# Performance work log

Hardware: AMD Instinct MI355X
Metric: run time of the kernel (lower is better)

The kernel has to match this reference:

```python
import jax, jax.numpy as jnp
import numpy as np

B, S, D, E = 8, 1024, 768, 8
F = 4 * D  # 3072


def setup_inputs() -> dict:
    key = jax.random.key(0)
    ks = jax.random.split(key, 5)
    scale = 0.02
    x = jax.random.normal(ks[0], (B, S, D), jnp.float32)
    gate_w = jax.random.normal(ks[1], (D, E), jnp.float32) * scale
    gate_b = jnp.zeros((E,), jnp.float32)
    w1 = jax.random.normal(ks[2], (E, D, F), jnp.float32) * scale
    b1 = jnp.zeros((E, F), jnp.float32)
    w2 = jax.random.normal(ks[3], (E, F, D), jnp.float32) * scale
    b2 = jnp.zeros((E, D), jnp.float32)
    return {"x": x, "gate_w": gate_w, "gate_b": gate_b,
            "w1": w1, "b1": b1, "w2": w2, "b2": b2}


def reference(x, gate_w, gate_b, w1, b1, w2, b2):
    # x: [B, S, D] -> tokens [T, D]
    orig_shape = x.shape
    xt = x.reshape(-1, x.shape[-1])  # [T, D]
    gates = jax.nn.softmax(xt @ gate_w + gate_b, axis=-1)  # [T, E]
    # original takes topk(k=2) but only uses indices[:, 0] == argmax (top-1)
    expert_idx = jnp.argmax(gates, axis=-1)  # [T]
    # NOTE: original does NOT scale expert output by gate probability.
    out = jnp.zeros_like(xt)
    n_experts = w1.shape[0]
    for e in range(n_experts):  # small fixed expert loop
        h = jax.nn.gelu(xt @ w1[e] + b1[e], approximate=False)  # [T, F]
        y = h @ w2[e] + b2[e]  # [T, D]
        out = jnp.where((expert_idx == e)[:, None], y, out)
    return out.reshape(orig_shape)
```

## Files before the change

### kernel.cpp

```cpp
#include <hip/hip_runtime.h>
#include <hip/hip_bf16.h>
#include <cstdint>
#include <cstddef>

static constexpr int T_TOK = 8192;
static constexpr int D_DIM = 768;
static constexpr int E_NUM = 8;
static constexpr int F_DIM = 3072;
static constexpr int MAX_TILES = 72;

typedef __attribute__((ext_vector_type(8))) short short8;
typedef __attribute__((ext_vector_type(4))) float floatx4;
typedef __attribute__((ext_vector_type(8))) unsigned short ushort8v;

__device__ __forceinline__ void async16(const void* g, void* l) {
  __builtin_amdgcn_global_load_lds(
      (const __attribute__((address_space(1))) unsigned int*)g,
      (__attribute__((address_space(3))) unsigned int*)l, 16, 0, 0);
}

__device__ __forceinline__ float gelu_fast(float v) {
  float s = v * (1.5957691f + 0.071354813f * v * v);
  return v / (1.0f + __expf(-s));
}

__global__ __launch_bounds__(256)
void gate_kernel(const float* __restrict__ x, const float* __restrict__ gw,
                 const float* __restrict__ gb, int* __restrict__ expert_idx,
                 __hip_bfloat16* __restrict__ xb) {
  int gid = blockIdx.x * blockDim.x + threadIdx.x;
  int tok = gid >> 6;
  int lane = threadIdx.x & 63;
  if (tok >= T_TOK) return;
  const float* xr = x + (size_t)tok * D_DIM;
  __hip_bfloat16* xbr = xb + (size_t)tok * D_DIM;
  float acc[8];
#pragma unroll
  for (int e = 0; e < 8; e++) acc[e] = 0.f;
#pragma unroll
  for (int i = 0; i < D_DIM / 64; i++) {
    int d = lane + i * 64;
    float v = xr[d];
    xbr[d] = __float2bfloat16(v);
    const float4* g4 = (const float4*)(gw + (size_t)d * 8);
    float4 a = g4[0], b = g4[1];
    acc[0] += v * a.x; acc[1] += v * a.y; acc[2] += v * a.z; acc[3] += v * a.w;
    acc[4] += v * b.x; acc[5] += v * b.y; acc[6] += v * b.z; acc[7] += v * b.w;
  }
#pragma unroll
  for (int e = 0; e < 8; e++) {
#pragma unroll
    for (int o = 32; o > 0; o >>= 1) acc[e] += __shfl_xor(acc[e], o, 64);
  }
  if (lane == 0) {
    int best = 0;
    float bv = acc[0] + gb[0];
#pragma unroll
    for (int e = 1; e < 8; e++) {
      float v = acc[e] + gb[e];
      if (v > bv) { bv = v; best = e; }
    }
    expert_idx[tok] = best;
  }
}

__global__ __launch_bounds__(256)
void count_kernel(const int* __restrict__ expert_idx, int* __restrict__ counts) {
  __shared__ int h[E_NUM];
  if (threadIdx.x < E_NUM) h[threadIdx.x] = 0;
  __syncthreads();
  int t = blockIdx.x * blockDim.x + threadIdx.x;
  if (t < T_TOK) atomicAdd(&h[expert_idx[t]], 1);
  __syncthreads();
  if (threadIdx.x < E_NUM && h[threadIdx.x] > 0)
    atomicAdd(&counts[threadIdx.x], h[threadIdx.x]);
}

__global__ void offsets_kernel(const int* __restrict__ counts, int* __restrict__ offs,
                               int* __restrict__ meta) {
  if (threadIdx.x == 0) {
    int s = 0, tc = 0;
    for (int e = 0; e < E_NUM; e++) {
      offs[e] = s;
      int cnt = counts[e];
      for (int m = 0; m * 128 < cnt; m++) {
        meta[1 + tc] = e;
        meta[1 + MAX_TILES + tc] = m;
        tc++;
      }
      s += cnt;
    }
    offs[E_NUM] = s;
    meta[0] = tc;
  }
}

__global__ __launch_bounds__(256)
void scatter_kernel(const int* __restrict__ expert_idx, const int* __restrict__ offs,
                    int* __restrict__ fill, int* __restrict__ perm) {
  __shared__ int lcnt[E_NUM];
  __shared__ int lbase[E_NUM];
  if (threadIdx.x < E_NUM) lcnt[threadIdx.x] = 0;
  __syncthreads();
  int t = blockIdx.x * blockDim.x + threadIdx.x;
  int e = -1, rank = 0;
  if (t < T_TOK) {
    e = expert_idx[t];
    rank = atomicAdd(&lcnt[e], 1);
  }
  __syncthreads();
  if (threadIdx.x < E_NUM)
    lbase[threadIdx.x] = (lcnt[threadIdx.x] > 0)
                           ? atomicAdd(&fill[threadIdx.x], lcnt[threadIdx.x]) : 0;
  __syncthreads();
  if (t < T_TOK) perm[offs[e] + lbase[e] + rank] = t;
}

__global__ __launch_bounds__(256)
void transpose_bf16(const float* __restrict__ in, __hip_bfloat16* __restrict__ out,
                    int R, int C) {
  __shared__ float t[64][65];
  const float* src = in + (size_t)blockIdx.z * R * C;
  __hip_bfloat16* dst = out + (size_t)blockIdx.z * R * C;
  int r0 = blockIdx.y * 64, c0 = blockIdx.x * 64;
  int tx = threadIdx.x & 15;
  int ty = threadIdx.x >> 4;
#pragma unroll
  for (int p = 0; p < 4; p++) {
    int r = ty + p * 16;
    float4 v = *(const float4*)&src[(size_t)(r0 + r) * C + c0 + tx * 4];
    t[tx * 4 + 0][r] = v.x; t[tx * 4 + 1][r] = v.y;
    t[tx * 4 + 2][r] = v.z; t[tx * 4 + 3][r] = v.w;
  }
  __syncthreads();
  int j = threadIdx.x & 7;
#pragma unroll
  for (int p = 0; p < 2; p++) {
    int cc = (threadIdx.x >> 3) + p * 32;
    __align__(16) __hip_bfloat16 tmp[8];
#pragma unroll
    for (int i = 0; i < 8; i++) tmp[i] = __float2bfloat16(t[cc][j * 8 + i]);
    *(ushort8v*)&dst[(size_t)(c0 + cc) * R + r0 + j * 8] = *(const ushort8v*)tmp;
  }
}

template<int K, int N, bool FIRST>
__global__ __launch_bounds__(256)
void moe_gemm(const __hip_bfloat16* __restrict__ A,
              const __hip_bfloat16* __restrict__ Bt,
              const float* __restrict__ bias,
              const int* __restrict__ meta,
              const int* __restrict__ offs,
              const int* __restrict__ perm,
              void* __restrict__ OutP) {
  int g = blockIdx.x;
  int xcd = g & 7;
  int j = g >> 3;
  int mt = xcd * 9 + (j % 9);
  int nt = j / 9;
  if (mt >= meta[0]) return;
  int e = meta[1 + mt];
  int m0 = meta[1 + MAX_TILES + mt] * 128;
  int off = offs[e], cnt = offs[e + 1] - off;
  int n0 = nt * 128;

  __shared__ __align__(16) __hip_bfloat16 As[3 * 4096];
  __shared__ __align__(16) __hip_bfloat16 Bs[3 * 4096];

  int tid = threadIdx.x, lane = tid & 63, w = tid >> 6;
  int lr0 = w * 32 + (lane >> 2), lr1 = lr0 + 16;
  int ch = (lane & 3) ^ ((lane >> 3) & 3);

  int r0 = m0 + lr0; if (r0 > cnt - 1) r0 = cnt - 1;
  int r1 = m0 + lr1; if (r1 > cnt - 1) r1 = cnt - 1;
  const __hip_bfloat16* a0;
  const __hip_bfloat16* a1;
  if constexpr (FIRST) {
    a0 = A + (size_t)perm[off + r0] * K + ch * 8;
    a1 = A + (size_t)perm[off + r1] * K + ch * 8;
  } else {
    a0 = A + (size_t)(off + r0) * K + ch * 8;
    a1 = A + (size_t)(off + r1) * K + ch * 8;
  }
  const __hip_bfloat16* Bbase = Bt + ((size_t)e * N + n0) * K;
  const __hip_bfloat16* bp0 = Bbase + (size_t)lr0 * K + ch * 8;
  const __hip_bfloat16* bp1 = Bbase + (size_t)lr1 * K + ch * 8;

  int wr = (w >> 1) * 64, wc = (w & 1) * 64;
  int mrow = lane & 15, cq = lane >> 4;
  int aoff[4], boff[4];
#pragma unroll
  for (int i = 0; i < 4; i++) {
    int rr = wr + i * 16 + mrow;
    aoff[i] = rr * 32 + ((cq ^ ((rr >> 1) & 3)) * 8);
    int rb = wc + i * 16 + mrow;
    boff[i] = rb * 32 + ((cq ^ ((rb >> 1) & 3)) * 8);
  }

  auto stage = [&](int slot, int ko) {
    __hip_bfloat16* la = &As[slot * 4096];
    __hip_bfloat16* lb = &Bs[slot * 4096];
    async16(a0 + ko, la + (w * 32) * 32);
    async16(a1 + ko, la + (w * 32 + 16) * 32);
    async16(bp0 + ko, lb + (w * 32) * 32);
    async16(bp1 + ko, lb + (w * 32 + 16) * 32);
  };

  floatx4 acc[4][4];
#pragma unroll
  for (int i = 0; i < 4; i++)
#pragma unroll
    for (int jj = 0; jj < 4; jj++) acc[i][jj] = (floatx4){0.f, 0.f, 0.f, 0.f};

  constexpr int NT = K / 32;
  stage(0, 0);
  stage(1, 32);
  for (int t = 0; t < NT; ++t) {
    if (t + 2 < NT) {
      stage((t + 2) % 3, (t + 2) * 32);
      asm volatile("s_waitcnt vmcnt(8)" ::: "memory");
    } else if (t + 1 < NT) {
      asm volatile("s_waitcnt vmcnt(4)" ::: "memory");
    } else {
      asm volatile("s_waitcnt vmcnt(0)" ::: "memory");
    }
    __builtin_amdgcn_s_barrier();
    __builtin_amdgcn_sched_barrier(0);
    int lb = (t % 3) * 4096;
    short8 af[4], bfv[4];
#pragma unroll
    for (int i = 0; i < 4; i++) af[i] = *(const short8*)&As[lb + aoff[i]];
#pragma unroll
    for (int i = 0; i < 4; i++) bfv[i] = *(const short8*)&Bs[lb + boff[i]];
#pragma unroll
    for (int mi = 0; mi < 4; mi++)
#pragma unroll
      for (int ni = 0; ni < 4; ni++)
        acc[mi][ni] = __builtin_amdgcn_mfma_f32_16x16x32_bf16(af[mi], bfv[ni], acc[mi][ni], 0, 0, 0);
    __builtin_amdgcn_sched_barrier(0);
    __builtin_amdgcn_s_barrier();
  }

#pragma unroll
  for (int mi = 0; mi < 4; mi++) {
    int rowl = wr + mi * 16 + (lane >> 4) * 4;
#pragma unroll
    for (int ni = 0; ni < 4; ni++) {
      int col = n0 + wc + ni * 16 + (lane & 15);
      float bia = bias[(size_t)e * N + col];
#pragma unroll
      for (int r = 0; r < 4; r++) {
        int gm = m0 + rowl + r;
        if (gm < cnt) {
          if constexpr (FIRST) {
            ((__hip_bfloat16*)OutP)[(size_t)(off + gm) * N + col] =
                __float2bfloat16(gelu_fast(acc[mi][ni][r] + bia));
          } else {
            ((float*)OutP)[(size_t)perm[off + gm] * N + col] = acc[mi][ni][r] + bia;
          }
        }
      }
    }
  }
}

extern "C" void kernel_launch(void* const* d_in, const int* in_sizes, int n_in,
                              void* d_out, int out_size, void* d_ws, size_t ws_size,
                              hipStream_t stream) {
  const float* x  = (const float*)d_in[0];
  const float* gw = (const float*)d_in[1];
  const float* gb = (const float*)d_in[2];
  const float* w1 = (const float*)d_in[3];
  const float* b1 = (const float*)d_in[4];
  const float* w2 = (const float*)d_in[5];
  const float* b2 = (const float*)d_in[6];
  float* out = (float*)d_out;

  char* ws = (char*)d_ws;
  int* counts = (int*)(ws + 0);
  int* fill   = (int*)(ws + 32);
  int* offs   = (int*)(ws + 64);
  int* meta   = (int*)(ws + 128);
  int* eidx   = (int*)(ws + 1024);
  int* perm   = (int*)(ws + 1024 + 4 * T_TOK);
  size_t off = 1024 + 8 * (size_t)T_TOK;
  __hip_bfloat16* xb  = (__hip_bfloat16*)(ws + off); off += (size_t)T_TOK * D_DIM * 2;
  __hip_bfloat16* w1t = (__hip_bfloat16*)(ws + off); off += (size_t)E_NUM * D_DIM * F_DIM * 2;
  __hip_bfloat16* w2t = (__hip_bfloat16*)(ws + off); off += (size_t)E_NUM * D_DIM * F_DIM * 2;
  __hip_bfloat16* H   = (__hip_bfloat16*)(ws + off); off += (size_t)T_TOK * F_DIM * 2;

  hipMemsetAsync(d_ws, 0, 64, stream);
  gate_kernel<<<T_TOK / 4, 256, 0, stream>>>(x, gw, gb, eidx, xb);
  count_kernel<<<T_TOK / 256, 256, 0, stream>>>(eidx, counts);
  offsets_kernel<<<1, 64, 0, stream>>>(counts, offs, meta);
  scatter_kernel<<<T_TOK / 256, 256, 0, stream>>>(eidx, offs, fill, perm);
  transpose_bf16<<<dim3(F_DIM / 64, D_DIM / 64, E_NUM), 256, 0, stream>>>(w1, w1t, D_DIM, F_DIM);
  transpose_bf16<<<dim3(D_DIM / 64, F_DIM / 64, E_NUM), 256, 0, stream>>>(w2, w2t, F_DIM, D_DIM);
  moe_gemm<D_DIM, F_DIM, true><<<8 * 9 * (F_DIM / 128), 256, 0, stream>>>(
      xb, w1t, b1, meta, offs, perm, (void*)H);
  moe_gemm<F_DIM, D_DIM, false><<<8 * 9 * (D_DIM / 128), 256, 0, stream>>>(
      H, w2t, b2, meta, offs, perm, (void*)out);
}
```

Measured before the change: 382.5 us.

## Widen first expert GEMM tile to 128x256 and vectorize gate kernel loads

Splits the templated MoE GEMM into two kernels. The first GEMM now uses a 128x256 output tile with a 4x8 MFMA accumulator per wave, so each A tile is reused across twice as many columns and the grid is halved. The gate kernel also switches to float4 loads of x and vectorized bf16 stores. The cost is higher register and LDS use in GEMM1, which may lower occupancy and give fewer blocks to spread across the CUs.

```diff
diff --git a/kernel.cpp b/kernel.cpp
--- a/kernel.cpp
+++ b/kernel.cpp
@@ -12,6 +12,7 @@
 typedef __attribute__((ext_vector_type(8))) short short8;
 typedef __attribute__((ext_vector_type(4))) float floatx4;
 typedef __attribute__((ext_vector_type(8))) unsigned short ushort8v;
+typedef __attribute__((ext_vector_type(4))) unsigned short ushort4v;
 
 __device__ __forceinline__ void async16(const void* g, void* l) {
   __builtin_amdgcn_global_load_lds(
@@ -38,14 +39,26 @@
 #pragma unroll
   for (int e = 0; e < 8; e++) acc[e] = 0.f;
 #pragma unroll
-  for (int i = 0; i < D_DIM / 64; i++) {
-    int d = lane + i * 64;
-    float v = xr[d];
-    xbr[d] = __float2bfloat16(v);
-    const float4* g4 = (const float4*)(gw + (size_t)d * 8);
-    float4 a = g4[0], b = g4[1];
-    acc[0] += v * a.x; acc[1] += v * a.y; acc[2] += v * a.z; acc[3] += v * a.w;
-    acc[4] += v * b.x; acc[5] += v * b.y; acc[6] += v * b.z; acc[7] += v * b.w;
+  for (int i = 0; i < 3; i++) {
+    int d0 = i * 256 + lane * 4;
+    float4 v = *(const float4*)&xr[d0];
+    __align__(8) __hip_bfloat16 tmp[4];
+    tmp[0] = __float2bfloat16(v.x); tmp[1] = __float2bfloat16(v.y);
+    tmp[2] = __float2bfloat16(v.z); tmp[3] = __float2bfloat16(v.w);
+    *(ushort4v*)&xbr[d0] = *(const ushort4v*)tmp;
+    const float4* g4 = (const float4*)(gw + (size_t)d0 * 8);
+    float4 a0 = g4[0], a1 = g4[1];
+    float4 b0 = g4[2], b1 = g4[3];
+    float4 c0 = g4[4], c1 = g4[5];
+    float4 e0 = g4[6], e1 = g4[7];
+    acc[0] += v.x * a0.x + v.y * b0.x + v.z * c0.x + v.w * e0.x;
+    acc[1] += v.x * a0.y + v.y * b0.y + v.z * c0.y + v.w * e0.y;
+    acc[2] += v.x * a0.z + v.y * b0.z + v.z * c0.z + v.w * e0.z;
+    acc[3] += v.x * a0.w + v.y * b0.w + v.z * c0.w + v.w * e0.w;
+    acc[4] += v.x * a1.x + v.y * b1.x + v.z * c1.x + v.w * e1.x;
+    acc[5] += v.x * a1.y + v.y * b1.y + v.z * c1.y + v.w * e1.y;
+    acc[6] += v.x * a1.z + v.y * b1.z + v.z * c1.z + v.w * e1.z;
+    acc[7] += v.x * a1.w + v.y * b1.w + v.z * c1.w + v.w * e1.w;
   }
 #pragma unroll
   for (int e = 0; e < 8; e++) {
@@ -144,15 +157,134 @@
   }
 }
 
-template<int K, int N, bool FIRST>
-__global__ __launch_bounds__(256)
-void moe_gemm(const __hip_bfloat16* __restrict__ A,
-              const __hip_bfloat16* __restrict__ Bt,
-              const float* __restrict__ bias,
-              const int* __restrict__ meta,
-              const int* __restrict__ offs,
-              const int* __restrict__ perm,
-              void* __restrict__ OutP) {
+__global__ __launch_bounds__(256)
+void moe_gemm1(const __hip_bfloat16* __restrict__ A,
+               const __hip_bfloat16* __restrict__ Bt,
+               const float* __restrict__ bias,
+               const int* __restrict__ meta,
+               const int* __restrict__ offs,
+               const int* __restrict__ perm,
+               __hip_bfloat16* __restrict__ H) {
+  constexpr int K = D_DIM, N = F_DIM;
+  constexpr int NT = K / 32;
+  int g = blockIdx.x;
+  int xcd = g & 7;
+  int j = g >> 3;
+  int mt = xcd * 9 + (j % 9);
+  int nt = j / 9;
+  if (mt >= meta[0]) return;
+  int e = meta[1 + mt];
+  int m0 = meta[1 + MAX_TILES + mt] * 128;
+  int off = offs[e], cnt = offs[e + 1] - off;
+  int n0 = nt * 256;
+
+  __shared__ __align__(16) __hip_bfloat16 As[3 * 4096];
+  __shared__ __align__(16) __hip_bfloat16 Bs[3 * 8192];
+
+  int tid = threadIdx.x, lane = tid & 63, w = tid >> 6;
+  int lr0 = w * 32 + (lane >> 2), lr1 = lr0 + 16;
+  int ch = (lane & 3) ^ ((lane >> 3) & 3);
+
+  int r0 = m0 + lr0; if (r0 > cnt - 1) r0 = cnt - 1;
+  int r1 = m0 + lr1; if (r1 > cnt - 1) r1 = cnt - 1;
+  const __hip_bfloat16* a0 = A + (size_t)perm[off + r0] * K + ch * 8;
+  const __hip_bfloat16* a1 = A + (size_t)perm[off + r1] * K + ch * 8;
+  const __hip_bfloat16* Bbase = Bt + ((size_t)e * N + n0) * K;
+  const __hip_bfloat16* bp0 = Bbase + (size_t)lr0 * K + ch * 8;
+  const __hip_bfloat16* bp1 = Bbase + (size_t)lr1 * K + ch * 8;
+  const __hip_bfloat16* bp2 = Bbase + (size_t)(128 + lr0) * K + ch * 8;
+  const __hip_bfloat16* bp3 = Bbase + (size_t)(128 + lr1) * K + ch * 8;
+
+  int wm = w >> 1, wn = w & 1;
+  int mrow = lane & 15, cq = lane >> 4;
+  int aoff[4], boff[8];
+#pragma unroll
+  for (int i = 0; i < 4; i++) {
+    int rr = wm * 64 + i * 16 + mrow;
+    aoff[i] = rr * 32 + ((cq ^ ((rr >> 1) & 3)) * 8);
+  }
+#pragma unroll
+  for (int i = 0; i < 8; i++) {
+    int rb = wn * 128 + i * 16 + mrow;
+    boff[i] = rb * 32 + ((cq ^ ((rb >> 1) & 3)) * 8);
+  }
+
+  auto stage = [&](int slot, int ko) {
+    __hip_bfloat16* la = &As[slot * 4096];
+    __hip_bfloat16* lb = &Bs[slot * 8192];
+    async16(a0 + ko, la + (w * 32) * 32);
+    async16(a1 + ko, la + (w * 32 + 16) * 32);
+    async16(bp0 + ko, lb + (w * 32) * 32);
+    async16(bp1 + ko, lb + (w * 32 + 16) * 32);
+    async16(bp2 + ko, lb + 4096 + (w * 32) * 32);
+    async16(bp3 + ko, lb + 4096 + (w * 32 + 16) * 32);
+  };
+
+  floatx4 acc[4][8];
+#pragma unroll
+  for (int i = 0; i < 4; i++)
+#pragma unroll
+    for (int jj = 0; jj < 8; jj++) acc[i][jj] = (floatx4){0.f, 0.f, 0.f, 0.f};
+
+  stage(0, 0);
+  stage(1, 32);
+  for (int t = 0; t < NT; ++t) {
+    if (t + 2 < NT) {
+      stage((t + 2) % 3, (t + 2) * 32);
+      asm volatile("s_waitcnt vmcnt(12)" ::: "memory");
+    } else if (t + 1 < NT) {
+      asm volatile("s_waitcnt vmcnt(6)" ::: "memory");
+    } else {
+      asm volatile("s_waitcnt vmcnt(0)" ::: "memory");
+    }
+    __builtin_amdgcn_s_barrier();
+    __builtin_amdgcn_sched_barrier(0);
+    int la_ = (t % 3) * 4096, lb_ = (t % 3) * 8192;
+    short8 af[4];
+#pragma unroll
+    for (int i = 0; i < 4; i++) af[i] = *(const short8*)&As[la_ + aoff[i]];
+#pragma unroll
+    for (int h = 0; h < 2; h++) {
+      short8 bfv[4];
+#pragma unroll
+      for (int cf = 0; cf < 4; cf++) bfv[cf] = *(const short8*)&Bs[lb_ + boff[h * 4 + cf]];
+#pragma unroll
+      for (int mi = 0; mi < 4; mi++)
+#pragma unroll
+        for (int cf = 0; cf < 4; cf++)
+          acc[mi][h * 4 + cf] =
+              __builtin_amdgcn_mfma_f32_16x16x32_bf16(af[mi], bfv[cf], acc[mi][h * 4 + cf], 0, 0, 0);
+    }
+    __builtin_amdgcn_sched_barrier(0);
+    __builtin_amdgcn_s_barrier();
+  }
+
+#pragma unroll
+  for (int mi = 0; mi < 4; mi++) {
+    int rowl = wm * 64 + mi * 16 + (lane >> 4) * 4;
+#pragma unroll
+    for (int ni = 0; ni < 8; ni++) {
+      int col = n0 + wn * 128 + ni * 16 + (lane & 15);
+      float bia = bias[(size_t)e * N + col];
+#pragma unroll
+      for (int r = 0; r < 4; r++) {
+        int gm = m0 + rowl + r;
+        if (gm < cnt)
+          H[(size_t)(off + gm) * N + col] = __float2bfloat16(gelu_fast(acc[mi][ni][r] + bia));
+      }
+    }
+  }
+}
+
+__global__ __launch_bounds__(256)
+void moe_gemm2(const __hip_bfloat16* __restrict__ A,
+               const __hip_bfloat16* __restrict__ Bt,
+               const float* __restrict__ bias,
+               const int* __restrict__ meta,
+               const int* __restrict__ offs,
+               const int* __restrict__ perm,
+               float* __restrict__ Out) {
+  constexpr int K = F_DIM, N = D_DIM;
   int g = blockIdx.x;
   int xcd = g & 7;
   int j = g >> 3;
@@ -173,15 +305,8 @@
 
   int r0 = m0 + lr0; if (r0 > cnt - 1) r0 = cnt - 1;
   int r1 = m0 + lr1; if (r1 > cnt - 1) r1 = cnt - 1;
-  const __hip_bfloat16* a0;
-  const __hip_bfloat16* a1;
-  if constexpr (FIRST) {
-    a0 = A + (size_t)perm[off + r0] * K + ch * 8;
-    a1 = A + (size_t)perm[off + r1] * K + ch * 8;
-  } else {
-    a0 = A + (size_t)(off + r0) * K + ch * 8;
-    a1 = A + (size_t)(off + r1) * K + ch * 8;
-  }
+  const __hip_bfloat16* a0 = A + (size_t)(off + r0) * K + ch * 8;
+  const __hip_bfloat16* a1 = A + (size_t)(off + r1) * K + ch * 8;
   const __hip_bfloat16* Bbase = Bt + ((size_t)e * N + n0) * K;
   const __hip_bfloat16* bp0 = Bbase + (size_t)lr0 * K + ch * 8;
   const __hip_bfloat16* bp1 = Bbase + (size_t)lr1 * K + ch * 8;
@@ -251,14 +376,8 @@
 #pragma unroll
       for (int r = 0; r < 4; r++) {
         int gm = m0 + rowl + r;
-        if (gm < cnt) {
-          if constexpr (FIRST) {
-            ((__hip_bfloat16*)OutP)[(size_t)(off + gm) * N + col] =
-                __float2bfloat16(gelu_fast(acc[mi][ni][r] + bia));
-          } else {
-            ((float*)OutP)[(size_t)perm[off + gm] * N + col] = acc[mi][ni][r] + bia;
-          }
-        }
+        if (gm < cnt)
+          Out[(size_t)perm[off + gm] * N + col] = acc[mi][ni][r] + bia;
       }
     }
   }
@@ -296,8 +415,6 @@
   scatter_kernel<<<T_TOK / 256, 256, 0, stream>>>(eidx, offs, fill, perm);
   transpose_bf16<<<dim3(F_DIM / 64, D_DIM / 64, E_NUM), 256, 0, stream>>>(w1, w1t, D_DIM, F_DIM);
   transpose_bf16<<<dim3(D_DIM / 64, F_DIM / 64, E_NUM), 256, 0, stream>>>(w2, w2t, F_DIM, D_DIM);
-  moe_gemm<D_DIM, F_DIM, true><<<8 * 9 * (F_DIM / 128), 256, 0, stream>>>(
-      xb, w1t, b1, meta, offs, perm, (void*)H);
-  moe_gemm<F_DIM, D_DIM, false><<<8 * 9 * (D_DIM / 128), 256, 0, stream>>>(
-      H, w2t, b2, meta, offs, perm, (void*)out);
-}
+  moe_gemm1<<<8 * 9 * (F_DIM / 256), 256, 0, stream>>>(xb, w1t, b1, meta, offs, perm, H);
+  moe_gemm2<<<8 * 9 * (D_DIM / 128), 256, 0, stream>>>(H, w2t, b2, meta, offs, perm, out);
+}
```

Result: slower. 400.2 us (+4.6%).
